# Performance work log

Measured on AMD Instinct MI355X. Metric: run time of the kernel, lower is better.

## Reference

```python
import jax, jax.numpy as jnp
import numpy as np

B, N, C_IN, C_OUT, CHEB_K, EMBED = 64, 2048, 64, 64, 3, 16


def setup_inputs() -> dict:
    key = jax.random.key(0)
    k1, k2, k3, k4 = jax.random.split(key, 4)
    return {
        "graph": 0,  # unused placeholder, matches original signature
        "node_feature": jax.random.normal(k1, (B, N, C_IN), dtype=jnp.float32),
        "node_embeddings": jax.random.normal(k2, (N, EMBED), dtype=jnp.float32),
        "weights_pool": jax.random.normal(k3, (EMBED, CHEB_K, C_IN, C_OUT), dtype=jnp.float32),
        "bias_pool": jax.random.normal(k4, (EMBED, C_OUT), dtype=jnp.float32),
    }


def reference(graph, node_feature, node_embeddings, weights_pool, bias_pool):
    x = node_feature                      # [B, N, C]
    n = node_embeddings.shape[0]
    # adaptive adjacency: softmax(relu(E E^T)) row-wise
    supports = jax.nn.softmax(jax.nn.relu(node_embeddings @ node_embeddings.T), axis=1)  # [N, N]
    # Chebyshev polynomial basis
    support_set = [jnp.eye(n, dtype=supports.dtype), supports]
    for _ in range(2, CHEB_K):
        support_set.append(2.0 * supports @ support_set[-1] - support_set[-2])
    supports_k = jnp.stack(support_set, axis=0)  # [K, N, N]
    # per-node dynamic weights / bias
    weights = jnp.einsum('nd,dkio->nkio', node_embeddings, weights_pool)  # [N, K, I, O]
    bias = node_embeddings @ bias_pool                                    # [N, O]
    # graph aggregation over Chebyshev orders
    x_g = jnp.einsum('knm,bmc->bnkc', supports_k, x)                      # [B, N, K, C]
    # per-node weighted contraction
    out = jnp.einsum('bnki,nkio->bno', x_g, weights) + bias               # [B, N, O]
    return out
```

## Files before the change

### kernel.cpp

```cpp
#include <hip/hip_runtime.h>
#include <hip/hip_bf16.h>

#define BB 64
#define NN 2048
#define CC 64
#define DD 16

typedef __attribute__((ext_vector_type(8))) short bf16x8;
typedef __attribute__((ext_vector_type(4))) float f32x4;

__device__ __forceinline__ ushort f2bf(float f) {
  unsigned u = __float_as_uint(f);
  u += 0x7fffu + ((u >> 16) & 1u);
  return (ushort)(u >> 16);
}
__device__ __forceinline__ float b2f(ushort h) {
  return __uint_as_float(((unsigned)h) << 16);
}

#define GLOAD16(g, l)                                                 \
  __builtin_amdgcn_global_load_lds(                                   \
      (const __attribute__((address_space(1))) void*)(g),             \
      (__attribute__((address_space(3))) void*)(l), 16, 0, 0)

__global__ __launch_bounds__(256) void transpose_x_kernel(
    const float* __restrict__ X, ushort* __restrict__ Xt) {
  const int b = blockIdx.y;
  const int m0 = blockIdx.x * 256;
  const int t = threadIdx.x;
  __shared__ ushort xs[256 * 64];

#pragma unroll
  for (int it = 0; it < 16; ++it) {
    const int idx = it * 256 + t;
    const int m = idx >> 4;
    const int cq = (idx & 15) * 4;
    float4 v = *(const float4*)&X[(size_t)b * NN * CC + (size_t)(m0 + m) * CC + cq];
    ushort4 h;
    h.x = f2bf(v.x); h.y = f2bf(v.y); h.z = f2bf(v.z); h.w = f2bf(v.w);
    *(ushort4*)((char*)xs + m * 128 + ((cq * 2) ^ ((m & 7) << 4))) = h;
  }
  __syncthreads();

  const int c = t >> 2;
  const int mb = (t & 3) * 64;
#pragma unroll
  for (int s = 0; s < 8; ++s) {
    unsigned w0 = 0, w1 = 0, w2 = 0, w3 = 0;
#pragma unroll
    for (int j = 0; j < 8; ++j) {
      const int m = mb + s * 8 + j;
      const ushort hv =
          *(const ushort*)((const char*)xs + m * 128 + ((2 * c) ^ ((m & 7) << 4)));
      const unsigned uv = (unsigned)hv << ((j & 1) * 16);
      if (j < 2) w0 |= uv; else if (j < 4) w1 |= uv;
      else if (j < 6) w2 |= uv; else w3 |= uv;
    }
    uint4 pk = {w0, w1, w2, w3};
    *(uint4*)&Xt[(size_t)b * CC * NN + (size_t)c * NN + m0 + mb + s * 8] = pk;
  }
}

__global__ __launch_bounds__(256) void wpt_kernel(
    const float* __restrict__ Wp, ushort* __restrict__ Wpt) {
  const int g = blockIdx.x * 256 + threadIdx.x;
  const int d = g / 1536;
  const int rem = g % 1536;
  const int o = rem / 24;
  const int ki0 = (rem % 24) * 8;
  bf16x8 h;
#pragma unroll
  for (int j = 0; j < 8; ++j)
    h[j] = (short)f2bf(Wp[d * 12288 + (ki0 + j) * 64 + o]);
  *(bf16x8*)&Wpt[d * 12288 + o * 192 + ki0] = h;
}

__global__ __launch_bounds__(256) void supports_kernel(
    const float* __restrict__ E, ushort* __restrict__ S) {
  const int n = blockIdx.x;
  const int t = threadIdx.x;

  __shared__ float en[DD];
  if (t < DD) en[t] = E[n * DD + t];
  __syncthreads();

  float e[DD];
#pragma unroll
  for (int d = 0; d < DD; ++d) e[d] = en[d];

  float vals[8];
  float vmax = 0.f;
#pragma unroll
  for (int j = 0; j < 8; ++j) {
    const int m = j * 256 + t;
    const float4* Em = (const float4*)&E[m * DD];
    float4 v0 = Em[0], v1 = Em[1], v2 = Em[2], v3 = Em[3];
    float dot = e[0]*v0.x + e[1]*v0.y + e[2]*v0.z + e[3]*v0.w
              + e[4]*v1.x + e[5]*v1.y + e[6]*v1.z + e[7]*v1.w
              + e[8]*v2.x + e[9]*v2.y + e[10]*v2.z + e[11]*v2.w
              + e[12]*v3.x + e[13]*v3.y + e[14]*v3.z + e[15]*v3.w;
    dot = fmaxf(dot, 0.f);
    vals[j] = dot;
    vmax = fmaxf(vmax, dot);
  }

  __shared__ float red[256];
  red[t] = vmax;
  __syncthreads();
  for (int s = 128; s > 0; s >>= 1) {
    if (t < s) red[t] = fmaxf(red[t], red[t + s]);
    __syncthreads();
  }
  vmax = red[0];
  __syncthreads();

  float sum = 0.f;
#pragma unroll
  for (int j = 0; j < 8; ++j) {
    vals[j] = __expf(vals[j] - vmax);
    sum += vals[j];
  }
  red[t] = sum;
  __syncthreads();
  for (int s = 128; s > 0; s >>= 1) {
    if (t < s) red[t] += red[t + s];
    __syncthreads();
  }
  const float inv = 1.f / red[0];

#pragma unroll
  for (int j = 0; j < 8; ++j)
    S[(size_t)n * NN + j * 256 + t] = f2bf(vals[j] * inv);
}

__global__ __launch_bounds__(256) void spmm_t_kernel(
    const ushort* __restrict__ At, const ushort* __restrict__ S,
    ushort* __restrict__ Yt, ushort* __restrict__ Yn) {
  const int b  = blockIdx.x;
  const int n0 = blockIdx.y * 256;
  const int t  = threadIdx.x;
  const int w  = t >> 6;
  const int l  = t & 63;

  __shared__ ushort Als[2][64 * 64];
  __shared__ ushort Bls[2][256 * 64];

  const char* Abase = (const char*)(At + (size_t)b * CC * NN);
  const char* Sbase = (const char*)S + (size_t)n0 * (NN * 2);

  f32x4 acc[4][4];
#pragma unroll
  for (int i = 0; i < 4; ++i)
#pragma unroll
    for (int j = 0; j < 4; ++j) acc[i][j] = (f32x4)0.f;

  const int lkb = (l & 7) * 16;
  const int lrw = w * 8 + (l >> 3);

  auto stage = [&](int buf, int mt) {
#pragma unroll
    for (int q = 0; q < 2; ++q) {
      const int row = q * 32 + lrw;
      GLOAD16(Abase + (size_t)row * (NN * 2) + mt * 2 + (lkb ^ ((row & 7) << 4)),
              (char*)Als[buf] + q * 4096 + w * 1024);
    }
#pragma unroll
    for (int q = 0; q < 8; ++q) {
      const int row = q * 32 + lrw;
      GLOAD16(Sbase + (size_t)row * (NN * 2) + mt * 2 + (lkb ^ ((row & 7) << 4)),
              (char*)Bls[buf] + q * 4096 + w * 1024);
    }
  };

  stage(0, 0);
  int cur = 0;
  for (int it = 0; it < 32; ++it) {
    const int nmt = ((it + 1) & 31) * 64;
    stage(cur ^ 1, nmt);
    asm volatile("s_waitcnt vmcnt(10)" ::: "memory");
    __builtin_amdgcn_s_barrier();
    __builtin_amdgcn_sched_barrier(0);

#pragma unroll
    for (int kk = 0; kk < 2; ++kk) {
      const int kb = kk * 64 + (l >> 4) * 16;
      bf16x8 a[4], bv[4];
#pragma unroll
      for (int cf = 0; cf < 4; ++cf) {
        const int c = cf * 16 + (l & 15);
        a[cf] = *(const bf16x8*)((const char*)Als[cur] + c * 128 +
                                 (kb ^ ((c & 7) << 4)));
      }
#pragma unroll
      for (int nf = 0; nf < 4; ++nf) {
        const int r = w * 64 + nf * 16 + (l & 15);
        bv[nf] = *(const bf16x8*)((const char*)Bls[cur] + r * 128 +
                                  (kb ^ ((r & 7) << 4)));
      }
#pragma unroll
      for (int cf = 0; cf < 4; ++cf)
#pragma unroll
        for (int nf = 0; nf < 4; ++nf)
          acc[cf][nf] = __builtin_amdgcn_mfma_f32_16x16x32_bf16(
              a[cf], bv[nf], acc[cf][nf], 0, 0, 0);
    }

    __builtin_amdgcn_sched_barrier(0);
    __builtin_amdgcn_s_barrier();
    cur ^= 1;
  }

  const int nw = n0 + w * 64;
#pragma unroll
  for (int cf = 0; cf < 4; ++cf) {
#pragma unroll
    for (int nf = 0; nf < 4; ++nf) {
      const int n = nw + nf * 16 + (l & 15);
      const int cb = cf * 16 + (l >> 4) * 4;
      ushort h0 = f2bf(acc[cf][nf][0]);
      ushort h1 = f2bf(acc[cf][nf][1]);
      ushort h2 = f2bf(acc[cf][nf][2]);
      ushort h3 = f2bf(acc[cf][nf][3]);
      if (Yt) {
        ushort* p = Yt + (size_t)b * CC * NN + (size_t)cb * NN + n;
        p[0] = h0; p[NN] = h1; p[2 * NN] = h2; p[3 * NN] = h3;
      }
      if (Yn) {
        ushort4 pk = {h0, h1, h2, h3};
        *(ushort4*)(Yn + (size_t)b * NN * CC + (size_t)n * CC + cb) = pk;
      }
    }
  }
}

__global__ __launch_bounds__(512) void out_kernel(
    const float* __restrict__ E, const ushort* __restrict__ Wpt,
    const float* __restrict__ Bp, const float* __restrict__ X,
    const ushort* __restrict__ Y1n, const ushort* __restrict__ Y1t,
    const ushort* __restrict__ Y2n, float* __restrict__ Out) {
  const int n0 = blockIdx.x * 2;
  const int t = threadIdx.x;

  __shared__ ushort Wt[2][64 * 192];
  __shared__ ushort xg[2][64 * 192];
  __shared__ float bsh[2][64];
  __shared__ float esh[2][DD];

  if (t < 2 * DD) esh[t >> 4][t & 15] = E[(n0 + (t >> 4)) * DD + (t & 15)];
  __syncthreads();
  float ea[DD], eb[DD];
#pragma unroll
  for (int d = 0; d < DD; ++d) { ea[d] = esh[0][d]; eb[d] = esh[1][d]; }

  if (t < 128) {
    const int node = t >> 6, o = t & 63;
    const float* e = node ? eb : ea;
    float bsum = 0.f;
#pragma unroll
    for (int d = 0; d < DD; ++d) bsum = fmaf(e[d], Bp[d * 64 + o], bsum);
    bsh[node][o] = bsum;
  }

#pragma unroll
  for (int it = 0; it < 3; ++it) {
    const int boff = it * 8192 + t * 16;
    float acc0[8] = {}, acc1[8] = {};
#pragma unroll
    for (int d = 0; d < DD; ++d) {
      bf16x8 wv = *(const bf16x8*)((const char*)Wpt + d * 24576 + boff);
#pragma unroll
      for (int u = 0; u < 8; ++u) {
        const float f = b2f((ushort)wv[u]);
        acc0[u] = fmaf(ea[d], f, acc0[u]);
        acc1[u] = fmaf(eb[d], f, acc1[u]);
      }
    }
    bf16x8 h0, h1;
#pragma unroll
    for (int u = 0; u < 8; ++u) {
      h0[u] = (short)f2bf(acc0[u]);
      h1[u] = (short)f2bf(acc1[u]);
    }
    const int o = boff / 384;
    const int sw = (boff % 384) ^ ((o & 7) << 4);
    *(bf16x8*)((char*)Wt[0] + o * 384 + sw) = h0;
    *(bf16x8*)((char*)Wt[1] + o * 384 + sw) = h1;
  }

  {
    const int node = t >> 8, tt = t & 255;
    const int b = tt >> 2, i0 = (tt & 3) * 16;
    const int n = n0 + node;
    const size_t NC = (size_t)NN * CC;
    const size_t gbase = (size_t)b * NC + (size_t)n * CC + i0;
    char* xgn = (char*)xg[node];
    float xv[16];
#pragma unroll
    for (int j = 0; j < 4; ++j) {
      float4 v = *(const float4*)&X[gbase + j * 4];
      xv[j * 4 + 0] = v.x; xv[j * 4 + 1] = v.y;
      xv[j * 4 + 2] = v.z; xv[j * 4 + 3] = v.w;
    }
#pragma unroll
    for (int h = 0; h < 2; ++h) {
      bf16x8 hv;
#pragma unroll
      for (int u = 0; u < 8; ++u) hv[u] = (short)f2bf(xv[h * 8 + u]);
      const int ki = i0 + h * 8;
      *(bf16x8*)(xgn + b * 384 + ((ki * 2) ^ ((b & 7) << 4))) = hv;
    }
    if (Y1n) {
#pragma unroll
      for (int h = 0; h < 2; ++h) {
        bf16x8 hv = *(const bf16x8*)&Y1n[gbase + h * 8];
        const int ki = 64 + i0 + h * 8;
        *(bf16x8*)(xgn + b * 384 + ((ki * 2) ^ ((b & 7) << 4))) = hv;
      }
    } else {
#pragma unroll
      for (int h = 0; h < 2; ++h) {
        bf16x8 hv;
#pragma unroll
        for (int u = 0; u < 8; ++u)
          hv[u] = (short)Y1t[(size_t)b * NC + (size_t)(i0 + h * 8 + u) * NN + n];
        const int ki = 64 + i0 + h * 8;
        *(bf16x8*)(xgn + b * 384 + ((ki * 2) ^ ((b & 7) << 4))) = hv;
      }
    }
#pragma unroll
    for (int h = 0; h < 2; ++h) {
      bf16x8 y2 = *(const bf16x8*)&Y2n[gbase + h * 8];
      bf16x8 hv;
#pragma unroll
      for (int u = 0; u < 8; ++u)
        hv[u] = (short)f2bf(2.f * b2f((ushort)y2[u]) - xv[h * 8 + u]);
      const int ki = 128 + i0 + h * 8;
      *(bf16x8*)(xgn + b * 384 + ((ki * 2) ^ ((b & 7) << 4))) = hv;
    }
  }
  __syncthreads();

  const int w8 = t >> 6, l = t & 63;
  const int node = w8 >> 2, q = w8 & 3;
  const int br = (q & 1) * 32, oc = (q >> 1) * 32;
  const char* xgn = (const char*)xg[node];
  const char* wtn = (const char*)Wt[node];

  f32x4 acc[2][2];
#pragma unroll
  for (int i = 0; i < 2; ++i)
#pragma unroll
    for (int j = 0; j < 2; ++j) acc[i][j] = (f32x4)0.f;

#pragma unroll
  for (int s = 0; s < 6; ++s) {
    const int kb = s * 64 + (l >> 4) * 16;
    bf16x8 av[2], bv[2];
#pragma unroll
    for (int i = 0; i < 2; ++i) {
      const int row = br + i * 16 + (l & 15);
      av[i] = *(const bf16x8*)(xgn + row * 384 + (kb ^ ((row & 7) << 4)));
    }
#pragma unroll
    for (int j = 0; j < 2; ++j) {
      const int row = oc + j * 16 + (l & 15);
      bv[j] = *(const bf16x8*)(wtn + row * 384 + (kb ^ ((row & 7) << 4)));
    }
#pragma unroll
    for (int i = 0; i < 2; ++i)
#pragma unroll
      for (int j = 0; j < 2; ++j)
        acc[i][j] = __builtin_amdgcn_mfma_f32_16x16x32_bf16(av[i], bv[j],
                                                            acc[i][j], 0, 0, 0);
  }

  const size_t NC = (size_t)NN * CC;
  const int n = n0 + node;
#pragma unroll
  for (int i = 0; i < 2; ++i) {
#pragma unroll
    for (int j = 0; j < 2; ++j) {
      const int o = oc + j * 16 + (l & 15);
      const int bb = br + i * 16 + (l >> 4) * 4;
      const float bo = bsh[node][o];
#pragma unroll
      for (int r = 0; r < 4; ++r)
        Out[(size_t)(bb + r) * NC + (size_t)n * CC + o] = acc[i][j][r] + bo;
    }
  }
}

extern "C" void kernel_launch(void* const* d_in, const int* in_sizes, int n_in,
                              void* d_out, int out_size, void* d_ws, size_t ws_size,
                              hipStream_t stream) {
  const float* x  = (const float*)d_in[1];
  const float* E  = (const float*)d_in[2];
  const float* Wp = (const float*)d_in[3];
  const float* Bp = (const float*)d_in[4];
  float* out = (float*)d_out;

  const size_t szS  = (size_t)NN * NN * 2;
  const size_t szY  = (size_t)BB * NN * CC * 2;
  const size_t szWp = (size_t)DD * 3 * CC * CC * 2;
  ushort* Sb  = (ushort*)d_ws;
  ushort* Xt  = (ushort*)((char*)d_ws + szS);
  ushort* Y1t = (ushort*)((char*)d_ws + szS + szY);
  ushort* Wpt = (ushort*)((char*)d_ws + szS + 2 * szY);
  ushort* Y1n = (ushort*)((char*)d_ws + szS + 2 * szY + szWp);
  ushort* Y2n = Xt;
  const bool haveY1n = ws_size >= szS + 3 * szY + szWp;

  transpose_x_kernel<<<dim3(NN / 256, BB), 256, 0, stream>>>(x, Xt);
  wpt_kernel<<<96, 256, 0, stream>>>(Wp, Wpt);
  supports_kernel<<<NN, 256, 0, stream>>>(E, Sb);

  dim3 g2(BB, NN / 256);
  spmm_t_kernel<<<g2, 256, 0, stream>>>(Xt, Sb, Y1t, haveY1n ? Y1n : nullptr);
  spmm_t_kernel<<<g2, 256, 0, stream>>>(Y1t, Sb, nullptr, Y2n);

  out_kernel<<<NN / 2, 512, 0, stream>>>(E, Wpt, Bp, x, haveY1n ? Y1n : nullptr,
                                         Y1t, Y2n, out);
}
```

Baseline: 172.8 us.

## Enlarge spmm tile to two batches per block with 512-thread 2x4 wave grid

Each spmm block now computes two batches (128 rows of the transposed activations) against a 256-column slice of the support matrix, using 8 waves in a 2x4 layout. This halves the number of blocks and so halves redundant reloads of the support tile S per batch, raising arithmetic intensity. The inner loop is also restructured to hold B fragments across both k-halves, split the A work into two halves, and raise wave priority around the MFMA bursts. The trade-offs are more LDS per block (48 KB), fewer blocks (256) for the GPU, and an adjusted vmcnt wait count.

```diff
diff --git a/kernel.cpp b/kernel.cpp
--- a/kernel.cpp
+++ b/kernel.cpp
@@ -133,19 +133,20 @@
     S[(size_t)n * NN + j * 256 + t] = f2bf(vals[j] * inv);
 }
 
-__global__ __launch_bounds__(256) void spmm_t_kernel(
+__global__ __launch_bounds__(512) void spmm_t_kernel(
     const ushort* __restrict__ At, const ushort* __restrict__ S,
     ushort* __restrict__ Yt, ushort* __restrict__ Yn) {
-  const int b  = blockIdx.x;
+  const int bm = blockIdx.x;
   const int n0 = blockIdx.y * 256;
   const int t  = threadIdx.x;
   const int w  = t >> 6;
   const int l  = t & 63;
-
-  __shared__ ushort Als[2][64 * 64];
+  const int wm = w >> 2, wn = w & 3;
+
+  __shared__ ushort Als[2][128 * 64];
   __shared__ ushort Bls[2][256 * 64];
 
-  const char* Abase = (const char*)(At + (size_t)b * CC * NN);
+  const char* Abase = (const char*)(At + (size_t)bm * 128 * NN);
   const char* Sbase = (const char*)S + (size_t)n0 * (NN * 2);
 
   f32x4 acc[4][4];
@@ -160,15 +161,15 @@
   auto stage = [&](int buf, int mt) {
 #pragma unroll
     for (int q = 0; q < 2; ++q) {
-      const int row = q * 32 + lrw;
+      const int row = q * 64 + lrw;
       GLOAD16(Abase + (size_t)row * (NN * 2) + mt * 2 + (lkb ^ ((row & 7) << 4)),
-              (char*)Als[buf] + q * 4096 + w * 1024);
-    }
-#pragma unroll
-    for (int q = 0; q < 8; ++q) {
-      const int row = q * 32 + lrw;
+              (char*)Als[buf] + q * 8192 + w * 1024);
+    }
+#pragma unroll
+    for (int q = 0; q < 4; ++q) {
+      const int row = q * 64 + lrw;
       GLOAD16(Sbase + (size_t)row * (NN * 2) + mt * 2 + (lkb ^ ((row & 7) << 4)),
-              (char*)Bls[buf] + q * 4096 + w * 1024);
+              (char*)Bls[buf] + q * 8192 + w * 1024);
     }
   };
 
@@ -177,32 +178,67 @@
   for (int it = 0; it < 32; ++it) {
     const int nmt = ((it + 1) & 31) * 64;
     stage(cur ^ 1, nmt);
-    asm volatile("s_waitcnt vmcnt(10)" ::: "memory");
+    __builtin_amdgcn_sched_barrier(0);
+    asm volatile("s_waitcnt vmcnt(6)" ::: "memory");
     __builtin_amdgcn_s_barrier();
     __builtin_amdgcn_sched_barrier(0);
 
-#pragma unroll
-    for (int kk = 0; kk < 2; ++kk) {
-      const int kb = kk * 64 + (l >> 4) * 16;
-      bf16x8 a[4], bv[4];
-#pragma unroll
-      for (int cf = 0; cf < 4; ++cf) {
-        const int c = cf * 16 + (l & 15);
-        a[cf] = *(const bf16x8*)((const char*)Als[cur] + c * 128 +
-                                 (kb ^ ((c & 7) << 4)));
-      }
-#pragma unroll
-      for (int nf = 0; nf < 4; ++nf) {
-        const int r = w * 64 + nf * 16 + (l & 15);
-        bv[nf] = *(const bf16x8*)((const char*)Bls[cur] + r * 128 +
-                                  (kb ^ ((r & 7) << 4)));
-      }
-#pragma unroll
-      for (int cf = 0; cf < 4; ++cf)
+    bf16x8 bfr[4][2];
+#pragma unroll
+    for (int nf = 0; nf < 4; ++nf) {
+      const int r = wn * 64 + nf * 16 + (l & 15);
+#pragma unroll
+      for (int kk = 0; kk < 2; ++kk) {
+        const int kb = kk * 64 + (l >> 4) * 16;
+        bfr[nf][kk] = *(const bf16x8*)((const char*)Bls[cur] + r * 128 +
+                                       (kb ^ ((r & 7) << 4)));
+      }
+    }
+    {
+      bf16x8 afr[2][2];
+#pragma unroll
+      for (int cf = 0; cf < 2; ++cf) {
+        const int row = wm * 64 + cf * 16 + (l & 15);
+#pragma unroll
+        for (int kk = 0; kk < 2; ++kk) {
+          const int kb = kk * 64 + (l >> 4) * 16;
+          afr[cf][kk] = *(const bf16x8*)((const char*)Als[cur] + row * 128 +
+                                         (kb ^ ((row & 7) << 4)));
+        }
+      }
+      __builtin_amdgcn_s_setprio(1);
+#pragma unroll
+      for (int cf = 0; cf < 2; ++cf)
 #pragma unroll
         for (int nf = 0; nf < 4; ++nf)
-          acc[cf][nf] = __builtin_amdgcn_mfma_f32_16x16x32_bf16(
-              a[cf], bv[nf], acc[cf][nf], 0, 0, 0);
+#pragma unroll
+          for (int kk = 0; kk < 2; ++kk)
+            acc[cf][nf] = __builtin_amdgcn_mfma_f32_16x16x32_bf16(
+                afr[cf][kk], bfr[nf][kk], acc[cf][nf], 0, 0, 0);
+      __builtin_amdgcn_s_setprio(0);
+    }
+    {
+      bf16x8 afr[2][2];
+#pragma unroll
+      for (int cf = 0; cf < 2; ++cf) {
+        const int row = wm * 64 + (cf + 2) * 16 + (l & 15);
+#pragma unroll
+        for (int kk = 0; kk < 2; ++kk) {
+          const int kb = kk * 64 + (l >> 4) * 16;
+          afr[cf][kk] = *(const bf16x8*)((const char*)Als[cur] + row * 128 +
+                                         (kb ^ ((row & 7) << 4)));
+        }
+      }
+      __builtin_amdgcn_s_setprio(1);
+#pragma unroll
+      for (int cf = 0; cf < 2; ++cf)
+#pragma unroll
+        for (int nf = 0; nf < 4; ++nf)
+#pragma unroll
+          for (int kk = 0; kk < 2; ++kk)
+            acc[cf + 2][nf] = __builtin_amdgcn_mfma_f32_16x16x32_bf16(
+                afr[cf][kk], bfr[nf][kk], acc[cf + 2][nf], 0, 0, 0);
+      __builtin_amdgcn_s_setprio(0);
     }
 
     __builtin_amdgcn_sched_barrier(0);
@@ -210,12 +246,12 @@
     cur ^= 1;
   }
 
-  const int nw = n0 + w * 64;
+  const int b = bm * 2 + wm;
 #pragma unroll
   for (int cf = 0; cf < 4; ++cf) {
 #pragma unroll
     for (int nf = 0; nf < 4; ++nf) {
-      const int n = nw + nf * 16 + (l & 15);
+      const int n = n0 + wn * 64 + nf * 16 + (l & 15);
       const int cb = cf * 16 + (l >> 4) * 4;
       ushort h0 = f2bf(acc[cf][nf][0]);
       ushort h1 = f2bf(acc[cf][nf][1]);
@@ -414,9 +450,9 @@
   wpt_kernel<<<96, 256, 0, stream>>>(Wp, Wpt);
   supports_kernel<<<NN, 256, 0, stream>>>(E, Sb);
 
-  dim3 g2(BB, NN / 256);
-  spmm_t_kernel<<<g2, 256, 0, stream>>>(Xt, Sb, Y1t, haveY1n ? Y1n : nullptr);
-  spmm_t_kernel<<<g2, 256, 0, stream>>>(Y1t, Sb, nullptr, Y2n);
+  dim3 g2(32, 8);
+  spmm_t_kernel<<<g2, 512, 0, stream>>>(Xt, Sb, Y1t, haveY1n ? Y1n : nullptr);
+  spmm_t_kernel<<<g2, 512, 0, stream>>>(Y1t, Sb, nullptr, Y2n);
 
   out_kernel<<<NN / 2, 512, 0, stream>>>(E, Wpt, Bp, x, haveY1n ? Y1n : nullptr,
                                          Y1t, Y2n, out);
```

Result: slower. 180.8 us (+4.6%).

## Store intermediates node-major and add direct MFMA output kernel reading global operands

Applied to the files above, without the earlier changes.

The transpose and SpMM kernels now also write bf16 copies of X, Y1 and Y2 in a node-major [N][B][C] layout. A new output kernel reads each node's batch slice straight from global memory into MFMA operands, with no staging into shared memory. It also computes the Chebyshev T2 = 2*Y2 - X term on the fly. The transposed Y1 buffer now lives in the output buffer, which frees workspace for the extra copies, at the cost of an additional bf16 write of X.

```diff
diff --git a/kernel.cpp b/kernel.cpp
--- a/kernel.cpp
+++ b/kernel.cpp
@@ -24,7 +24,8 @@
       (__attribute__((address_space(3))) void*)(l), 16, 0, 0)
 
 __global__ __launch_bounds__(256) void transpose_x_kernel(
-    const float* __restrict__ X, ushort* __restrict__ Xt) {
+    const float* __restrict__ X, ushort* __restrict__ Xt,
+    ushort* __restrict__ Xnb) {
   const int b = blockIdx.y;
   const int m0 = blockIdx.x * 256;
   const int t = threadIdx.x;
@@ -39,6 +40,8 @@
     ushort4 h;
     h.x = f2bf(v.x); h.y = f2bf(v.y); h.z = f2bf(v.z); h.w = f2bf(v.w);
     *(ushort4*)((char*)xs + m * 128 + ((cq * 2) ^ ((m & 7) << 4))) = h;
+    if (Xnb)
+      *(ushort4*)&Xnb[((size_t)(m0 + m) * BB + b) * CC + cq] = h;
   }
   __syncthreads();
 
@@ -135,7 +138,7 @@
 
 __global__ __launch_bounds__(256) void spmm_t_kernel(
     const ushort* __restrict__ At, const ushort* __restrict__ S,
-    ushort* __restrict__ Yt, ushort* __restrict__ Yn) {
+    ushort* __restrict__ Yt, ushort* __restrict__ Yn, int nb) {
   const int b  = blockIdx.x;
   const int n0 = blockIdx.y * 256;
   const int t  = threadIdx.x;
@@ -227,8 +230,134 @@
       }
       if (Yn) {
         ushort4 pk = {h0, h1, h2, h3};
-        *(ushort4*)(Yn + (size_t)b * NN * CC + (size_t)n * CC + cb) = pk;
-      }
+        if (nb)
+          *(ushort4*)(Yn + ((size_t)n * BB + b) * CC + cb) = pk;
+        else
+          *(ushort4*)(Yn + ((size_t)b * NN + n) * CC + cb) = pk;
+      }
+    }
+  }
+}
+
+__global__ __launch_bounds__(512) void out_kernel_direct(
+    const float* __restrict__ E, const ushort* __restrict__ Wpt,
+    const float* __restrict__ Bp, const ushort* __restrict__ Xnb,
+    const ushort* __restrict__ Y1nb, const ushort* __restrict__ Y2nb,
+    float* __restrict__ Out) {
+  const int n0 = blockIdx.x * 2;
+  const int t = threadIdx.x;
+
+  __shared__ ushort Wt[2][64 * 192];
+  __shared__ float bsh[2][64];
+  __shared__ float esh[2][DD];
+
+  if (t < 2 * DD) esh[t >> 4][t & 15] = E[(n0 + (t >> 4)) * DD + (t & 15)];
+  __syncthreads();
+  float ea[DD], eb[DD];
+#pragma unroll
+  for (int d = 0; d < DD; ++d) { ea[d] = esh[0][d]; eb[d] = esh[1][d]; }
+
+  if (t < 128) {
+    const int node = t >> 6, o = t & 63;
+    const float* e = node ? eb : ea;
+    float bsum = 0.f;
+#pragma unroll
+    for (int d = 0; d < DD; ++d) bsum = fmaf(e[d], Bp[d * 64 + o], bsum);
+    bsh[node][o] = bsum;
+  }
+
+#pragma unroll
+  for (int it = 0; it < 3; ++it) {
+    const int boff = it * 8192 + t * 16;
+    float acc0[8] = {}, acc1[8] = {};
+#pragma unroll
+    for (int d = 0; d < DD; ++d) {
+      bf16x8 wv = *(const bf16x8*)((const char*)Wpt + d * 24576 + boff);
+#pragma unroll
+      for (int u = 0; u < 8; ++u) {
+        const float f = b2f((ushort)wv[u]);
+        acc0[u] = fmaf(ea[d], f, acc0[u]);
+        acc1[u] = fmaf(eb[d], f, acc1[u]);
+      }
+    }
+    bf16x8 h0, h1;
+#pragma unroll
+    for (int u = 0; u < 8; ++u) {
+      h0[u] = (short)f2bf(acc0[u]);
+      h1[u] = (short)f2bf(acc1[u]);
+    }
+    const int o = boff / 384;
+    const int sw = (boff % 384) ^ ((o & 7) << 4);
+    *(bf16x8*)((char*)Wt[0] + o * 384 + sw) = h0;
+    *(bf16x8*)((char*)Wt[1] + o * 384 + sw) = h1;
+  }
+  __syncthreads();
+
+  const int w8 = t >> 6, l = t & 63;
+  const int node = w8 >> 2, q = w8 & 3;
+  const int br = (q & 1) * 32, oc = (q >> 1) * 32;
+  const int n = n0 + node;
+  const char* wtn = (const char*)Wt[node];
+  const ushort* xsrc  = Xnb  + (size_t)n * BB * CC;
+  const ushort* y1src = Y1nb + (size_t)n * BB * CC;
+  const ushort* y2src = Y2nb + (size_t)n * BB * CC;
+  const int kq = (l >> 4) * 8;
+
+  f32x4 acc[2][2];
+#pragma unroll
+  for (int i = 0; i < 2; ++i)
+#pragma unroll
+    for (int j = 0; j < 2; ++j) acc[i][j] = (f32x4)0.f;
+
+#pragma unroll
+  for (int s = 0; s < 6; ++s) {
+    const int kk = s >> 1;
+    const int ich = (s & 1) * 32 + kq;
+    bf16x8 av[2];
+#pragma unroll
+    for (int i = 0; i < 2; ++i) {
+      const int b = br + i * 16 + (l & 15);
+      const int off = b * CC + ich;
+      if (kk == 0) {
+        av[i] = *(const bf16x8*)&xsrc[off];
+      } else if (kk == 1) {
+        av[i] = *(const bf16x8*)&y1src[off];
+      } else {
+        bf16x8 y2 = *(const bf16x8*)&y2src[off];
+        bf16x8 xv = *(const bf16x8*)&xsrc[off];
+        bf16x8 hv;
+#pragma unroll
+        for (int u = 0; u < 8; ++u)
+          hv[u] = (short)f2bf(2.f * b2f((ushort)y2[u]) - b2f((ushort)xv[u]));
+        av[i] = hv;
+      }
+    }
+    bf16x8 bv[2];
+    const int kb = s * 64 + (l >> 4) * 16;
+#pragma unroll
+    for (int j = 0; j < 2; ++j) {
+      const int row = oc + j * 16 + (l & 15);
+      bv[j] = *(const bf16x8*)(wtn + row * 384 + (kb ^ ((row & 7) << 4)));
+    }
+#pragma unroll
+    for (int i = 0; i < 2; ++i)
+#pragma unroll
+      for (int j = 0; j < 2; ++j)
+        acc[i][j] = __builtin_amdgcn_mfma_f32_16x16x32_bf16(av[i], bv[j],
+                                                            acc[i][j], 0, 0, 0);
+  }
+
+  const size_t NC = (size_t)NN * CC;
+#pragma unroll
+  for (int i = 0; i < 2; ++i) {
+#pragma unroll
+    for (int j = 0; j < 2; ++j) {
+      const int o = oc + j * 16 + (l & 15);
+      const int bb = br + i * 16 + (l >> 4) * 4;
+      const float bo = bsh[node][o];
+#pragma unroll
+      for (int r = 0; r < 4; ++r)
+        Out[(size_t)(bb + r) * NC + (size_t)n * CC + o] = acc[i][j][r] + bo;
     }
   }
 }
@@ -404,20 +533,29 @@
   const size_t szWp = (size_t)DD * 3 * CC * CC * 2;
   ushort* Sb  = (ushort*)d_ws;
   ushort* Xt  = (ushort*)((char*)d_ws + szS);
-  ushort* Y1t = (ushort*)((char*)d_ws + szS + szY);
-  ushort* Wpt = (ushort*)((char*)d_ws + szS + 2 * szY);
-  ushort* Y1n = (ushort*)((char*)d_ws + szS + 2 * szY + szWp);
-  ushort* Y2n = Xt;
-  const bool haveY1n = ws_size >= szS + 3 * szY + szWp;
-
-  transpose_x_kernel<<<dim3(NN / 256, BB), 256, 0, stream>>>(x, Xt);
+  ushort* Wpt = (ushort*)((char*)d_ws + szS + szY);
+  char*   P   = (char*)d_ws + szS + szY + szWp;
+  ushort* Y1t = (ushort*)d_out;
+  ushort* Y2  = Xt;
+
+  const bool direct = ws_size >= szS + 3 * szY + szWp;
+
+  ushort* Xnb  = direct ? (ushort*)P : nullptr;
+  ushort* Y1nb = direct ? (ushort*)(P + szY) : nullptr;
+  ushort* Y1n  = direct ? nullptr : (ushort*)P;
+
+  transpose_x_kernel<<<dim3(NN / 256, BB), 256, 0, stream>>>(x, Xt, Xnb);
   wpt_kernel<<<96, 256, 0, stream>>>(Wp, Wpt);
   supports_kernel<<<NN, 256, 0, stream>>>(E, Sb);
 
   dim3 g2(BB, NN / 256);
-  spmm_t_kernel<<<g2, 256, 0, stream>>>(Xt, Sb, Y1t, haveY1n ? Y1n : nullptr);
-  spmm_t_kernel<<<g2, 256, 0, stream>>>(Y1t, Sb, nullptr, Y2n);
-
-  out_kernel<<<NN / 2, 512, 0, stream>>>(E, Wpt, Bp, x, haveY1n ? Y1n : nullptr,
-                                         Y1t, Y2n, out);
-}
+  spmm_t_kernel<<<g2, 256, 0, stream>>>(Xt, Sb, Y1t,
+                                        direct ? Y1nb : Y1n, direct ? 1 : 0);
+  spmm_t_kernel<<<g2, 256, 0, stream>>>(Y1t, Sb, nullptr, Y2, direct ? 1 : 0);
+
+  if (direct)
+    out_kernel_direct<<<NN / 2, 512, 0, stream>>>(E, Wpt, Bp, Xnb, Y1nb, Y2,
+                                                  out);
+  else
+    out_kernel<<<NN / 2, 512, 0, stream>>>(E, Wpt, Bp, x, Y1n, Y1t, Y2, out);
+}
```

Result: slower. 180.5 us (+4.4%).

## Halve spmm block to 128 threads with larger per-wave tiles and single LDS buffer

Applied to the files above, without the earlier changes.

The spmm kernel now runs with two waves per block instead of four. Each wave computes a 64x128 output tile instead of 64x64, which doubles the accumulator registers and improves reuse of A fragments. Double buffering in LDS is dropped: a single buffer is loaded after the compute barrier and waited on with vmcnt(0). This halves LDS use so more blocks can fit per CU, but it removes the overlap of loads with compute inside a block and adds register pressure.

```diff
diff --git a/kernel.cpp b/kernel.cpp
--- a/kernel.cpp
+++ b/kernel.cpp
@@ -133,7 +133,7 @@
     S[(size_t)n * NN + j * 256 + t] = f2bf(vals[j] * inv);
 }
 
-__global__ __launch_bounds__(256) void spmm_t_kernel(
+__global__ __launch_bounds__(128) void spmm_t_kernel(
     const ushort* __restrict__ At, const ushort* __restrict__ S,
     ushort* __restrict__ Yt, ushort* __restrict__ Yn) {
   const int b  = blockIdx.x;
@@ -142,79 +142,80 @@
   const int w  = t >> 6;
   const int l  = t & 63;
 
-  __shared__ ushort Als[2][64 * 64];
-  __shared__ ushort Bls[2][256 * 64];
+  __shared__ ushort Als[64 * 64];
+  __shared__ ushort Bls[256 * 64];
 
   const char* Abase = (const char*)(At + (size_t)b * CC * NN);
   const char* Sbase = (const char*)S + (size_t)n0 * (NN * 2);
 
-  f32x4 acc[4][4];
+  f32x4 acc[4][8];
 #pragma unroll
   for (int i = 0; i < 4; ++i)
 #pragma unroll
-    for (int j = 0; j < 4; ++j) acc[i][j] = (f32x4)0.f;
+    for (int j = 0; j < 8; ++j) acc[i][j] = (f32x4)0.f;
 
   const int lkb = (l & 7) * 16;
   const int lrw = w * 8 + (l >> 3);
 
-  auto stage = [&](int buf, int mt) {
-#pragma unroll
-    for (int q = 0; q < 2; ++q) {
-      const int row = q * 32 + lrw;
+  auto stage = [&](int mt) {
+#pragma unroll
+    for (int q = 0; q < 4; ++q) {
+      const int row = q * 16 + lrw;
       GLOAD16(Abase + (size_t)row * (NN * 2) + mt * 2 + (lkb ^ ((row & 7) << 4)),
-              (char*)Als[buf] + q * 4096 + w * 1024);
-    }
-#pragma unroll
-    for (int q = 0; q < 8; ++q) {
-      const int row = q * 32 + lrw;
+              (char*)Als + q * 2048 + w * 1024);
+    }
+#pragma unroll
+    for (int q = 0; q < 16; ++q) {
+      const int row = q * 16 + lrw;
       GLOAD16(Sbase + (size_t)row * (NN * 2) + mt * 2 + (lkb ^ ((row & 7) << 4)),
-              (char*)Bls[buf] + q * 4096 + w * 1024);
+              (char*)Bls + q * 2048 + w * 1024);
     }
   };
 
-  stage(0, 0);
-  int cur = 0;
+  stage(0);
   for (int it = 0; it < 32; ++it) {
-    const int nmt = ((it + 1) & 31) * 64;
-    stage(cur ^ 1, nmt);
-    asm volatile("s_waitcnt vmcnt(10)" ::: "memory");
+    asm volatile("s_waitcnt vmcnt(0)" ::: "memory");
     __builtin_amdgcn_s_barrier();
     __builtin_amdgcn_sched_barrier(0);
 
 #pragma unroll
     for (int kk = 0; kk < 2; ++kk) {
       const int kb = kk * 64 + (l >> 4) * 16;
-      bf16x8 a[4], bv[4];
+      bf16x8 a[4];
 #pragma unroll
       for (int cf = 0; cf < 4; ++cf) {
         const int c = cf * 16 + (l & 15);
-        a[cf] = *(const bf16x8*)((const char*)Als[cur] + c * 128 +
+        a[cf] = *(const bf16x8*)((const char*)Als + c * 128 +
                                  (kb ^ ((c & 7) << 4)));
       }
 #pragma unroll
-      for (int nf = 0; nf < 4; ++nf) {
-        const int r = w * 64 + nf * 16 + (l & 15);
-        bv[nf] = *(const bf16x8*)((const char*)Bls[cur] + r * 128 +
-                                  (kb ^ ((r & 7) << 4)));
-      }
-#pragma unroll
-      for (int cf = 0; cf < 4; ++cf)
-#pragma unroll
-        for (int nf = 0; nf < 4; ++nf)
-          acc[cf][nf] = __builtin_amdgcn_mfma_f32_16x16x32_bf16(
-              a[cf], bv[nf], acc[cf][nf], 0, 0, 0);
+      for (int ng = 0; ng < 2; ++ng) {
+        bf16x8 bv[4];
+#pragma unroll
+        for (int nf = 0; nf < 4; ++nf) {
+          const int r = w * 128 + ng * 64 + nf * 16 + (l & 15);
+          bv[nf] = *(const bf16x8*)((const char*)Bls + r * 128 +
+                                    (kb ^ ((r & 7) << 4)));
+        }
+#pragma unroll
+        for (int cf = 0; cf < 4; ++cf)
+#pragma unroll
+          for (int nf = 0; nf < 4; ++nf)
+            acc[cf][ng * 4 + nf] = __builtin_amdgcn_mfma_f32_16x16x32_bf16(
+                a[cf], bv[nf], acc[cf][ng * 4 + nf], 0, 0, 0);
+      }
     }
 
     __builtin_amdgcn_sched_barrier(0);
     __builtin_amdgcn_s_barrier();
-    cur ^= 1;
-  }
-
-  const int nw = n0 + w * 64;
+    if (it < 31) stage((it + 1) * 64);
+  }
+
+  const int nw = n0 + w * 128;
 #pragma unroll
   for (int cf = 0; cf < 4; ++cf) {
 #pragma unroll
-    for (int nf = 0; nf < 4; ++nf) {
+    for (int nf = 0; nf < 8; ++nf) {
       const int n = nw + nf * 16 + (l & 15);
       const int cb = cf * 16 + (l >> 4) * 4;
       ushort h0 = f2bf(acc[cf][nf][0]);
@@ -415,8 +416,8 @@
   supports_kernel<<<NN, 256, 0, stream>>>(E, Sb);
 
   dim3 g2(BB, NN / 256);
-  spmm_t_kernel<<<g2, 256, 0, stream>>>(Xt, Sb, Y1t, haveY1n ? Y1n : nullptr);
-  spmm_t_kernel<<<g2, 256, 0, stream>>>(Y1t, Sb, nullptr, Y2n);
+  spmm_t_kernel<<<g2, 128, 0, stream>>>(Xt, Sb, Y1t, haveY1n ? Y1n : nullptr);
+  spmm_t_kernel<<<g2, 128, 0, stream>>>(Y1t, Sb, nullptr, Y2n);
 
   out_kernel<<<NN / 2, 512, 0, stream>>>(E, Wpt, Bp, x, haveY1n ? Y1n : nullptr,
                                          Y1t, Y2n, out);
```

After: 188.3 us. +8.9%, slower.
